# Kernel tuning notes

Hardware: AMD Instinct MI355X
Metric: run time of the kernel (lower is better)

## Reference

```python
import jax, jax.numpy as jnp
import numpy as np

T, B, DZ, DH, DS = 1000, 256, 64, 256, 16


def setup_inputs() -> dict:
    key = jax.random.key(0)
    k = jax.random.split(key, 6)
    r_w1 = 1.0 / np.sqrt(DZ)   # init_uniform_same: r = 1/sqrt(last dim)
    r_w2 = 1.0 / np.sqrt(DH)
    r_c = 1.0 / np.sqrt(DS)
    # W_trial=True: same initial matrix repeated across trials
    W1 = jnp.tile(jax.random.uniform(k[0], (DH, DZ), minval=-r_w1, maxval=r_w1), (B, 1, 1))
    W2 = jnp.tile(jax.random.uniform(k[1], (DZ, DH), minval=-r_w2, maxval=r_w2), (B, 1, 1))
    C = jax.random.uniform(k[2], (DZ, DS), minval=-r_c, maxval=r_c)
    A = jnp.full((DZ,), 0.95, dtype=jnp.float32)
    h1 = jax.random.normal(k[3], (DH,), dtype=jnp.float32)
    h2 = jax.random.normal(k[4], (DZ,), dtype=jnp.float32)
    kz, ks = jax.random.split(k[5])
    z0 = jax.random.normal(kz, (B, DZ), dtype=jnp.float32)
    s = jax.random.normal(ks, (T, B, DS), dtype=jnp.float32) * 0.1
    return {"z0": z0, "s": s, "A": A, "W1": W1, "W2": W2, "h1": h1, "h2": h2, "C": C}


def reference(z0, s, A, W1, W2, h1, h2, C):
    # Precompute external-input projection for all steps: s_t @ C.T  -> [T, B, DZ]
    Cs = jnp.einsum('tbs,zs->tbz', s, C)

    def step(z, cs_t):
        # per-trial W1: Wz = einsum('ij,ijk->ik', z, W1^T) == einsum('bj,bhj->bh', z, W1)
        Wz = jnp.einsum('bj,bhj->bh', z, W1)                       # [B, DH]
        z_act = jax.nn.relu(Wz + h1) - jax.nn.relu(Wz)             # clipped shPLRNN nonlinearity
        z_new = A * z + jnp.einsum('bh,bzh->bz', z_act, W2) + h2 + cs_t
        return z_new, z_new

    _, z_seq = jax.lax.scan(step, z0, Cs)  # z_seq: [T, B, DZ]
    return z_seq
```

## Files before the change

### kernel.cpp

```cpp
#include <hip/hip_runtime.h>

#define T_STEPS 1000
#define NB 256
#define DZ 64
#define DH 256
#define DS 16
#define CHUNK 64
#define NCHUNK 16

__device__ __forceinline__ void barrier_lgkm() {
    asm volatile("s_waitcnt lgkmcnt(0)\n\ts_barrier" ::: "memory");
}

template<int CTRL>
__device__ __forceinline__ float dpp_add(float x) {
    int y = __builtin_amdgcn_update_dpp(0, __float_as_int(x), CTRL, 0xF, 0xF, true);
    return x + __int_as_float(y);
}
__device__ __forceinline__ float row16_allsum(float x) {
    x = dpp_add<0x128>(x);
    x = dpp_add<0x124>(x);
    x = dpp_add<0x122>(x);
    x = dpp_add<0x121>(x);
    return x;
}

__global__ __launch_bounds__(1024)
__attribute__((amdgpu_waves_per_eu(4, 4)))
void plrnn_scan(const float* __restrict__ z0, const float* __restrict__ s,
                const float* __restrict__ A,  const float* __restrict__ W1,
                const float* __restrict__ W2, const float* __restrict__ h1,
                const float* __restrict__ h2, const float* __restrict__ C,
                float* __restrict__ out)
{
    const int tid = threadIdx.x;
    const int b   = blockIdx.x;
    const int h   = tid >> 2;
    const int q   = tid & 3;
    const int j   = tid >> 4;
    const int r4  = tid & 15;

    __shared__ __align__(16) float z_sh[DZ];
    __shared__ __align__(16) float za_sh[320];
    __shared__ __align__(16) float s_sh[CHUNK * DS];

    float4 w1v[4];
    {
        const float4* p = (const float4*)(W1 + (size_t)b * DH * DZ) + 4 * tid;
        #pragma unroll
        for (int k = 0; k < 4; ++k) w1v[k] = p[k];
    }
    float4 w2v[4];
    {
        const float4* p = (const float4*)(W2 + (size_t)b * DZ * DH) + 4 * tid;
        #pragma unroll
        for (int k = 0; k < 4; ++k) w2v[k] = p[k];
    }
    const float cj  = C[tid];

    const float h1r  = h1[h];
    const float rsgn = (h1r > 0.f) ?  1.f : -1.f;
    const float roff = (h1r > 0.f) ?  h1r :  0.f;
    const float rlo  = fminf(h1r, 0.f);
    const float rhi  = fmaxf(h1r, 0.f);

    const float Aj    = A[j];
    const float h2j16 = h2[j] * 0.0625f;
    float zr = z0[b * DZ + j];

    if (tid < DZ) z_sh[tid] = z0[b * DZ + tid];

    const int srow = tid >> 4, scol = tid & 15;
    float sreg = s[(size_t)min(srow, T_STEPS - 1) * NB * DS + (size_t)b * DS + scol];

    const int zi = h + ((h >> 4) << 2);
    float* outp = out + (size_t)b * DZ + j;

    __syncthreads();

    for (int ci = 0; ci < NCHUNK; ++ci) {
        const int t0 = ci * CHUNK;
        const int nt = (ci == NCHUNK - 1) ? (T_STEPS - t0) : CHUNK;
        s_sh[tid] = sreg;
        {
            int tl = min(t0 + CHUNK + srow, T_STEPS - 1);
            sreg = s[(size_t)tl * NB * DS + (size_t)b * DS + scol];
        }

        #pragma unroll 4
        for (int tt = 0; tt < nt; ++tt) {
            const float4* z4 = (const float4*)(z_sh + 16 * q);
            float a0 = 0.f, a1 = 0.f, a2 = 0.f, a3 = 0.f;
            #pragma unroll
            for (int k = 0; k < 4; ++k) {
                float4 zv = z4[k];
                a0 = fmaf(w1v[k].x, zv.x, a0);
                a1 = fmaf(w1v[k].y, zv.y, a1);
                a2 = fmaf(w1v[k].z, zv.z, a2);
                a3 = fmaf(w1v[k].w, zv.w, a3);
            }
            float p1 = (a0 + a1) + (a2 + a3);
            p1 = dpp_add<0xB1>(p1);
            p1 = dpp_add<0x4E>(p1);
            float za = __builtin_amdgcn_fmed3f(fmaf(rsgn, p1, roff), rlo, rhi);
            if (q == 0) za_sh[zi] = za;
            barrier_lgkm();

            const float4* q4 = (const float4*)(za_sh + 20 * r4);
            float sv = s_sh[tt * DS + r4];
            float p00 = fmaf(cj, sv, h2j16);
            float p01 = 0.f, p02 = 0.f, p03 = 0.f;
            #pragma unroll
            for (int k = 0; k < 4; ++k) {
                float4 v = q4[k];
                p00 = fmaf(w2v[k].x, v.x, p00);
                p01 = fmaf(w2v[k].y, v.y, p01);
                p02 = fmaf(w2v[k].z, v.z, p02);
                p03 = fmaf(w2v[k].w, v.w, p03);
            }
            float pa = (p00 + p01) + (p02 + p03);
            pa = row16_allsum(pa);

            float zn = fmaf(Aj, zr, pa);
            zr = zn;
            if (r4 == 0) {
                z_sh[j] = zn;
                *outp = zn;
            }
            outp += NB * DZ;
            barrier_lgkm();
        }
    }
}

extern "C" void kernel_launch(void* const* d_in, const int* in_sizes, int n_in,
                              void* d_out, int out_size, void* d_ws, size_t ws_size,
                              hipStream_t stream) {
    const float* z0p = (const float*)d_in[0];
    const float* sp  = (const float*)d_in[1];
    const float* Ap  = (const float*)d_in[2];
    const float* W1p = (const float*)d_in[3];
    const float* W2p = (const float*)d_in[4];
    const float* h1p = (const float*)d_in[5];
    const float* h2p = (const float*)d_in[6];
    const float* Cp  = (const float*)d_in[7];

    plrnn_scan<<<dim3(NB), dim3(1024), 0, stream>>>(z0p, sp, Ap, W1p, W2p, h1p, h2p, Cp,
                                                    (float*)d_out);
}
```

Before: 571.3 us.

## Remap weight layout so each lane computes four outputs with transpose-reduce shuffles

Weights are redistributed so each thread holds four output rows times a four-wide slice of the reduction dimension. Partial sums are combined with a quad transpose-sum using DPP moves, which replaces per-output butterfly reductions with fewer cross-lane operations per output. The second matvec now reduces across a full wave using DPP, ds_swizzle and ds_bpermute, and the shared za buffer loses its padding. The change trades reduction shuffles for broadcast LDS reads and adds higher-latency swizzle/bpermute steps to the serial dependency chain.

```diff
diff --git a/kernel.cpp b/kernel.cpp
--- a/kernel.cpp
+++ b/kernel.cpp
@@ -13,16 +13,21 @@
 }
 
 template<int CTRL>
-__device__ __forceinline__ float dpp_add(float x) {
-    int y = __builtin_amdgcn_update_dpp(0, __float_as_int(x), CTRL, 0xF, 0xF, true);
-    return x + __int_as_float(y);
+__device__ __forceinline__ float dpp_mov(float x) {
+    return __int_as_float(
+        __builtin_amdgcn_update_dpp(0, __float_as_int(x), CTRL, 0xF, 0xF, true));
 }
-__device__ __forceinline__ float row16_allsum(float x) {
-    x = dpp_add<0x128>(x);
-    x = dpp_add<0x124>(x);
-    x = dpp_add<0x122>(x);
-    x = dpp_add<0x121>(x);
-    return x;
+template<int CTRL>
+__device__ __forceinline__ float dpp_add(float x) { return x + dpp_mov<CTRL>(x); }
+
+__device__ __forceinline__ float quad_transpose_sum(float p0, float p1, float p2,
+                                                    float p3, bool b1, bool b2) {
+    float rA = dpp_mov<0xB1>(b1 ? p0 : p1);
+    float uA = (b1 ? p1 : p0) + rA;
+    float rB = dpp_mov<0xB1>(b1 ? p2 : p3);
+    float uB = (b1 ? p3 : p2) + rB;
+    float rC = dpp_mov<0x4E>(b2 ? uA : uB);
+    return (b2 ? uB : uA) + rC;
 }
 
 __global__ __launch_bounds__(1024)
@@ -35,46 +40,55 @@
 {
     const int tid = threadIdx.x;
     const int b   = blockIdx.x;
-    const int h   = tid >> 2;
-    const int q   = tid & 3;
-    const int j   = tid >> 4;
+    const int qq  = tid & 3;
+    const bool b1 = (tid & 1) != 0;
+    const bool b2 = (tid & 2) != 0;
     const int r4  = tid & 15;
+    const int g1  = tid >> 4;
+    const int wv  = tid >> 6;
+    const int l   = tid & 63;
+    const int d   = (tid >> 2) & 15;
 
     __shared__ __align__(16) float z_sh[DZ];
-    __shared__ __align__(16) float za_sh[320];
+    __shared__ __align__(16) float za_sh[DH];
     __shared__ __align__(16) float s_sh[CHUNK * DS];
 
     float4 w1v[4];
     {
-        const float4* p = (const float4*)(W1 + (size_t)b * DH * DZ) + 4 * tid;
+        const float* base = W1 + (size_t)b * DH * DZ + 4 * r4;
         #pragma unroll
-        for (int k = 0; k < 4; ++k) w1v[k] = p[k];
+        for (int m = 0; m < 4; ++m)
+            w1v[m] = *(const float4*)(base + (size_t)(4 * g1 + m) * DZ);
     }
     float4 w2v[4];
     {
-        const float4* p = (const float4*)(W2 + (size_t)b * DZ * DH) + 4 * tid;
+        const float* base = W2 + (size_t)b * DZ * DH + 4 * l;
         #pragma unroll
-        for (int k = 0; k < 4; ++k) w2v[k] = p[k];
+        for (int m = 0; m < 4; ++m)
+            w2v[m] = *(const float4*)(base + (size_t)(4 * wv + m) * DH);
     }
-    const float cj  = C[tid];
 
-    const float h1r  = h1[h];
+    const int   hsel = 4 * g1 + qq;
+    const float h1r  = h1[hsel];
     const float rsgn = (h1r > 0.f) ?  1.f : -1.f;
     const float roff = (h1r > 0.f) ?  h1r :  0.f;
     const float rlo  = fminf(h1r, 0.f);
     const float rhi  = fmaxf(h1r, 0.f);
 
-    const float Aj    = A[j];
-    const float h2j16 = h2[j] * 0.0625f;
-    float zr = z0[b * DZ + j];
+    const int   jsel  = 4 * wv + qq;
+    const float Aj    = A[jsel];
+    const float h2j16 = h2[jsel] * 0.0625f;
+    const float cj    = C[jsel * DS + d];
+    float zr = z0[b * DZ + jsel];
+
+    const int bpi = (l ^ 32) << 2;
 
     if (tid < DZ) z_sh[tid] = z0[b * DZ + tid];
 
     const int srow = tid >> 4, scol = tid & 15;
     float sreg = s[(size_t)min(srow, T_STEPS - 1) * NB * DS + (size_t)b * DS + scol];
 
-    const int zi = h + ((h >> 4) << 2);
-    float* outp = out + (size_t)b * DZ + j;
+    float* outp = out + (size_t)b * DZ + jsel;
 
     __syncthreads();
 
@@ -89,42 +103,44 @@
 
         #pragma unroll 4
         for (int tt = 0; tt < nt; ++tt) {
-            const float4* z4 = (const float4*)(z_sh + 16 * q);
-            float a0 = 0.f, a1 = 0.f, a2 = 0.f, a3 = 0.f;
-            #pragma unroll
-            for (int k = 0; k < 4; ++k) {
-                float4 zv = z4[k];
-                a0 = fmaf(w1v[k].x, zv.x, a0);
-                a1 = fmaf(w1v[k].y, zv.y, a1);
-                a2 = fmaf(w1v[k].z, zv.z, a2);
-                a3 = fmaf(w1v[k].w, zv.w, a3);
-            }
-            float p1 = (a0 + a1) + (a2 + a3);
-            p1 = dpp_add<0xB1>(p1);
-            p1 = dpp_add<0x4E>(p1);
-            float za = __builtin_amdgcn_fmed3f(fmaf(rsgn, p1, roff), rlo, rhi);
-            if (q == 0) za_sh[zi] = za;
+            float4 zv = *(const float4*)(z_sh + 4 * r4);
+            float a0 = w1v[0].x * zv.x, a1 = w1v[1].x * zv.x,
+                  a2 = w1v[2].x * zv.x, a3 = w1v[3].x * zv.x;
+            a0 = fmaf(w1v[0].y, zv.y, a0); a1 = fmaf(w1v[1].y, zv.y, a1);
+            a2 = fmaf(w1v[2].y, zv.y, a2); a3 = fmaf(w1v[3].y, zv.y, a3);
+            a0 = fmaf(w1v[0].z, zv.z, a0); a1 = fmaf(w1v[1].z, zv.z, a1);
+            a2 = fmaf(w1v[2].z, zv.z, a2); a3 = fmaf(w1v[3].z, zv.z, a3);
+            a0 = fmaf(w1v[0].w, zv.w, a0); a1 = fmaf(w1v[1].w, zv.w, a1);
+            a2 = fmaf(w1v[2].w, zv.w, a2); a3 = fmaf(w1v[3].w, zv.w, a3);
+            float t1 = quad_transpose_sum(a0, a1, a2, a3, b1, b2);
+            t1 = dpp_add<0x124>(t1);
+            t1 = dpp_add<0x128>(t1);
+            float za = __builtin_amdgcn_fmed3f(fmaf(rsgn, t1, roff), rlo, rhi);
+            if (r4 < 4) za_sh[4 * g1 + r4] = za;
             barrier_lgkm();
 
-            const float4* q4 = (const float4*)(za_sh + 20 * r4);
-            float sv = s_sh[tt * DS + r4];
-            float p00 = fmaf(cj, sv, h2j16);
-            float p01 = 0.f, p02 = 0.f, p03 = 0.f;
-            #pragma unroll
-            for (int k = 0; k < 4; ++k) {
-                float4 v = q4[k];
-                p00 = fmaf(w2v[k].x, v.x, p00);
-                p01 = fmaf(w2v[k].y, v.y, p01);
-                p02 = fmaf(w2v[k].z, v.z, p02);
-                p03 = fmaf(w2v[k].w, v.w, p03);
-            }
-            float pa = (p00 + p01) + (p02 + p03);
-            pa = row16_allsum(pa);
-
-            float zn = fmaf(Aj, zr, pa);
+            float4 av = *(const float4*)(za_sh + 4 * l);
+            float sv = s_sh[tt * DS + d];
+            float p0 = w2v[0].x * av.x, p1 = w2v[1].x * av.x,
+                  p2 = w2v[2].x * av.x, p3 = w2v[3].x * av.x;
+            p0 = fmaf(w2v[0].y, av.y, p0); p1 = fmaf(w2v[1].y, av.y, p1);
+            p2 = fmaf(w2v[2].y, av.y, p2); p3 = fmaf(w2v[3].y, av.y, p3);
+            p0 = fmaf(w2v[0].z, av.z, p0); p1 = fmaf(w2v[1].z, av.z, p1);
+            p2 = fmaf(w2v[2].z, av.z, p2); p3 = fmaf(w2v[3].z, av.z, p3);
+            p0 = fmaf(w2v[0].w, av.w, p0); p1 = fmaf(w2v[1].w, av.w, p1);
+            p2 = fmaf(w2v[2].w, av.w, p2); p3 = fmaf(w2v[3].w, av.w, p3);
+            float pm = quad_transpose_sum(p0, p1, p2, p3, b1, b2);
+            pm += fmaf(cj, sv, h2j16);
+            pm = dpp_add<0x124>(pm);
+            pm = dpp_add<0x128>(pm);
+            pm += __int_as_float(__builtin_amdgcn_ds_swizzle(
+                      __float_as_int(pm), 0x401F));
+            pm += __int_as_float(__builtin_amdgcn_ds_bpermute(
+                      bpi, __float_as_int(pm)));
+            float zn = fmaf(Aj, zr, pm);
             zr = zn;
-            if (r4 == 0) {
-                z_sh[j] = zn;
+            if (l < 4) {
+                z_sh[4 * wv + l] = zn;
                 *outp = zn;
             }
             outp += NB * DZ;
```

New measurement: 668.1 us. +16.9%, slower.
